# Performance work log

Hardware: AMD Instinct MI355X
Metric: run time of the kernel (lower is better)

The kernel has to match this reference:

```python
import jax, jax.numpy as jnp
import numpy as np

B, S, HID = 4, 2048, 512
NH, HD = 8, 64
MAX_REL = 512


def setup_inputs() -> dict:
    key = jax.random.key(0)
    ks = jax.random.split(key, 10)
    sd = 0.02
    return {
        "hidden_states": jax.random.normal(ks[0], (B, S, HID), jnp.float32),
        "attention_mask": jnp.ones((B, S), jnp.float32),
        "Wq": jax.random.normal(ks[1], (HID, HID), jnp.float32) * sd,
        "bq": jnp.zeros((HID,), jnp.float32),
        "Wk": jax.random.normal(ks[2], (HID, HID), jnp.float32) * sd,
        "bk": jnp.zeros((HID,), jnp.float32),
        "Wv": jax.random.normal(ks[3], (HID, HID), jnp.float32) * sd,
        "bv": jnp.zeros((HID,), jnp.float32),
        "Wo": jax.random.normal(ks[4], (HID, HID), jnp.float32) * sd,
        "bo": jnp.zeros((HID,), jnp.float32),
        "rel_table": jax.random.normal(ks[5], (2 * MAX_REL + 1, NH), jnp.float32) * sd,
    }


def _heads(x):
    # [B,S,HID] -> [B,NH,S,HD]
    return x.reshape(B, S, NH, HD).transpose(0, 2, 1, 3)


def reference(hidden_states, attention_mask, Wq, bq, Wk, bk, Wv, bv, Wo, bo, rel_table):
    q = _heads(hidden_states @ Wq + bq)
    k = _heads(hidden_states @ Wk + bk)
    v = _heads(hidden_states @ Wv + bv)

    scores = jnp.einsum("bhqd,bhkd->bhqk", q, k) / jnp.sqrt(jnp.float32(HD))

    # relative position bias: rel[i,j] = clip(j-i, -MAX_REL, MAX_REL) + MAX_REL
    pos = jnp.arange(S)
    rel = jnp.clip(pos[None, :] - pos[:, None], -MAX_REL, MAX_REL) + MAX_REL
    bias = rel_table[rel]                      # [S,S,NH]
    bias = bias.transpose(2, 0, 1)             # [NH,S,S]
    scores = scores + bias[None]

    # mask: 1 attend, 0 masked
    neg = jnp.finfo(scores.dtype).min
    scores = scores + (1.0 - attention_mask)[:, None, None, :] * neg

    probs = jax.nn.softmax(scores, axis=-1)
    ctx = jnp.einsum("bhqk,bhkd->bhqd", probs, v)
    ctx = ctx.transpose(0, 2, 1, 3).reshape(B, S, HID)
    return ctx @ Wo + bo
```

## Files before the change

### kernel.cpp

```cpp
#include <hip/hip_runtime.h>
#include <hip/hip_bf16.h>

#define B_    4
#define S_    2048
#define HID_  512
#define NH_   8
#define HD_   64
#define MAXREL 512
#define M_    (B_ * S_)

#define LOG2E 1.44269504f
#define SCALE_Q (0.125f * LOG2E)

typedef __attribute__((ext_vector_type(8))) short bf8;
typedef __attribute__((ext_vector_type(4))) float f4;
typedef __attribute__((ext_vector_type(16))) float f16f;

static __device__ __forceinline__ unsigned short f2bf(float f) {
    union { float f; unsigned int u; } v; v.f = f;
    unsigned int u = v.u;
    unsigned int r = (u + 0x7FFFu + ((u >> 16) & 1u)) >> 16;
    return (unsigned short)r;
}

static __device__ __forceinline__ float ex2(float x) {
    float r; asm("v_exp_f32 %0, %1" : "=v"(r) : "v"(x)); return r;
}

static __device__ __forceinline__ void gload16(const void* g, void* l) {
    __builtin_amdgcn_global_load_lds(
        (const __attribute__((address_space(1))) unsigned int*)g,
        (__attribute__((address_space(3))) unsigned int*)l, 16, 0, 0);
}

static __device__ __forceinline__ bf8 mkbf8(unsigned a, unsigned b, unsigned c, unsigned d) {
    uint4 u = make_uint4(a, b, c, d);
    return *(bf8*)&u;
}

#define MFMA16(a, b, c) __builtin_amdgcn_mfma_f32_16x16x32_bf16((a), (b), (c), 0, 0, 0)
#define MFMA32(a, b, c) __builtin_amdgcn_mfma_f32_32x32x16_bf16((a), (b), (c), 0, 0, 0)

__global__ void k_cast_hs(const float* __restrict__ src, unsigned short* __restrict__ dst, int n4) {
    int i = blockIdx.x * blockDim.x + threadIdx.x;
    if (i >= n4) return;
    float4 v = ((const float4*)src)[i];
    ushort4 o;
    o.x = f2bf(v.x); o.y = f2bf(v.y); o.z = f2bf(v.z); o.w = f2bf(v.w);
    ((ushort4*)dst)[i] = o;
}

__global__ void k_prep_mask(const float* __restrict__ mask, float* __restrict__ maskadd) {
    int i = blockIdx.x * blockDim.x + threadIdx.x;
    if (i < M_) maskadd[i] = (1.0f - mask[i]) * -3.0e38f;
}

__global__ void k_transpose_w4(const float* __restrict__ W0, const float* __restrict__ W1,
                               const float* __restrict__ W2, const float* __restrict__ W3,
                               unsigned short* __restrict__ T0, unsigned short* __restrict__ T1,
                               unsigned short* __restrict__ T2, unsigned short* __restrict__ T3) {
    __shared__ float tile[32][33];
    const int z = blockIdx.z;
    const float* W = (z == 0) ? W0 : (z == 1) ? W1 : (z == 2) ? W2 : W3;
    unsigned short* T = (z == 0) ? T0 : (z == 1) ? T1 : (z == 2) ? T2 : T3;
    const int tx = threadIdx.x & 31, ty = threadIdx.x >> 5;
    const int n0 = blockIdx.x * 32, k0 = blockIdx.y * 32;
    #pragma unroll
    for (int i = 0; i < 4; ++i)
        tile[ty + i * 8][tx] = W[(size_t)(k0 + ty + i * 8) * HID_ + n0 + tx];
    __syncthreads();
    #pragma unroll
    for (int i = 0; i < 4; ++i)
        T[(size_t)(n0 + ty + i * 8) * HID_ + k0 + tx] = f2bf(tile[tx][ty + i * 8]);
}

__global__ __launch_bounds__(256, 3) void k_gemm_qkv(
    const unsigned short* __restrict__ Abf,
    const unsigned short* __restrict__ Wqt, const unsigned short* __restrict__ Wkt,
    const unsigned short* __restrict__ Wvt,
    const float* __restrict__ bq, const float* __restrict__ bk, const float* __restrict__ bv,
    unsigned short* __restrict__ Q, unsigned short* __restrict__ K, unsigned short* __restrict__ Vt)
{
    __shared__ unsigned short Al[2][128 * 32];
    __shared__ unsigned short Bl[2][128 * 32];

    const int t = threadIdx.x;
    const int lane = t & 63, w = t >> 6;
    const int lr = lane & 15, lg = lane >> 4;
    const int wr = w >> 1, wc = w & 1;

    const int m0 = blockIdx.x * 128;
    const int ng = blockIdx.y * 128;
    const int z = ng >> 9;
    const int n0 = ng & 511;
    const unsigned short* Wt = (z == 0) ? Wqt : ((z == 1) ? Wkt : Wvt);
    const float* bias = (z == 0) ? bq : ((z == 1) ? bk : bv);
    const float osc = (z == 0) ? SCALE_Q : 1.0f;

    const int srow = t >> 2;
    const int sc = (((t & 3) ^ ((srow >> 1) & 3))) * 8;
    const unsigned short* Ag0 = &Abf[(size_t)(m0 + srow) * HID_ + sc];
    const unsigned short* Ag1 = &Abf[(size_t)(m0 + 64 + srow) * HID_ + sc];
    const unsigned short* Bg0 = &Wt[(size_t)(n0 + srow) * HID_ + sc];
    const unsigned short* Bg1 = &Wt[(size_t)(n0 + 64 + srow) * HID_ + sc];
    char* dA0 = (char*)&Al[0][0] + w * 1024;
    char* dB0 = (char*)&Bl[0][0] + w * 1024;

    const int fx = (lr >> 1) & 3;
    int aoff[4], boff[4];
    #pragma unroll
    for (int i = 0; i < 4; ++i) {
        aoff[i] = (wr * 64 + i * 16 + lr) * 32 + ((lg ^ fx) * 8);
        boff[i] = (wc * 64 + i * 16 + lr) * 32 + ((lg ^ fx) * 8);
    }

    gload16(Ag0, dA0);
    gload16(Ag1, dA0 + 4096);
    gload16(Bg0, dB0);
    gload16(Bg1, dB0 + 4096);
    __syncthreads();

    f4 acc[4][4] = {};
    for (int kt = 0; kt < 16; ++kt) {
        const int cur = kt & 1;
        if (kt < 15) {
            const int ko = (kt + 1) * 32;
            const int bo = (cur ^ 1) * 8192;
            gload16(Ag0 + ko, dA0 + bo);
            gload16(Ag1 + ko, dA0 + bo + 4096);
            gload16(Bg0 + ko, dB0 + bo);
            gload16(Bg1 + ko, dB0 + bo + 4096);
        }
        bf8 af[4], bf_[4];
        #pragma unroll
        for (int i = 0; i < 4; ++i) {
            af[i]  = *(const bf8*)&Al[cur][aoff[i]];
            bf_[i] = *(const bf8*)&Bl[cur][boff[i]];
        }
        #pragma unroll
        for (int mi = 0; mi < 4; ++mi)
            #pragma unroll
            for (int ni = 0; ni < 4; ++ni)
                acc[mi][ni] = MFMA16(af[mi], bf_[ni], acc[mi][ni]);
        __syncthreads();
    }

    #pragma unroll
    for (int mi = 0; mi < 4; ++mi)
    #pragma unroll
    for (int ni = 0; ni < 4; ++ni) {
        const int col = n0 + wc * 64 + ni * 16 + lr;
        const int h = col >> 6, d = col & 63;
        const float bs = bias[col];
        const int row0 = m0 + wr * 64 + mi * 16 + lg * 4;
        const int b = row0 >> 11, s0 = row0 & 2047;
        if (z == 2) {
            ushort4 o;
            o.x = f2bf(acc[mi][ni][0] + bs);
            o.y = f2bf(acc[mi][ni][1] + bs);
            o.z = f2bf(acc[mi][ni][2] + bs);
            o.w = f2bf(acc[mi][ni][3] + bs);
            *(ushort4*)&Vt[(((size_t)(b * NH_ + h)) * HD_ + d) * S_ + s0] = o;
        } else {
            unsigned short* dst = (z == 0) ? Q : K;
            #pragma unroll
            for (int r = 0; r < 4; ++r) {
                float v = (acc[mi][ni][r] + bs) * osc;
                dst[(((size_t)(b * NH_ + h)) * S_ + s0 + r) * HD_ + d] = f2bf(v);
            }
        }
    }
}

__global__ __launch_bounds__(512) void k_gemm_out(
    const unsigned short* __restrict__ Abf,
    const unsigned short* __restrict__ Wot,
    const float* __restrict__ bo,
    float* __restrict__ out)
{
    __shared__ unsigned short Al[2][128 * 32];
    __shared__ unsigned short Bl[2][128 * 32];

    const int t = threadIdx.x;
    const int lane = t & 63, w = t >> 6;
    const int lr = lane & 15, lg = lane >> 4;
    const int wr = w >> 2, wc = w & 3;

    const int m0 = blockIdx.x * 128;
    const int n0 = blockIdx.y * 128;

    const int srow = t >> 2;
    const int sc = (((t & 3) ^ ((srow >> 1) & 3))) * 8;
    const unsigned short* Ag = &Abf[(size_t)(m0 + srow) * HID_ + sc];
    const unsigned short* Bg = &Wot[(size_t)(n0 + srow) * HID_ + sc];
    char* dA = (char*)&Al[0][0] + w * 1024;
    char* dB = (char*)&Bl[0][0] + w * 1024;

    const int fx = (lr >> 1) & 3;
    int aoff[4], boff[2];
    #pragma unroll
    for (int i = 0; i < 4; ++i)
        aoff[i] = (wr * 64 + i * 16 + lr) * 32 + ((lg ^ fx) * 8);
    #pragma unroll
    for (int i = 0; i < 2; ++i)
        boff[i] = (wc * 32 + i * 16 + lr) * 32 + ((lg ^ fx) * 8);

    gload16(Ag, dA);
    gload16(Bg, dB);
    __syncthreads();

    f4 acc[4][2] = {};
    for (int kt = 0; kt < 16; ++kt) {
        const int cur = kt & 1;
        if (kt < 15) {
            const int ko = (kt + 1) * 32;
            const int bo_ = (cur ^ 1) * 8192;
            gload16(Ag + ko, dA + bo_);
            gload16(Bg + ko, dB + bo_);
        }
        bf8 af[4], bf_[2];
        #pragma unroll
        for (int i = 0; i < 4; ++i) af[i] = *(const bf8*)&Al[cur][aoff[i]];
        #pragma unroll
        for (int i = 0; i < 2; ++i) bf_[i] = *(const bf8*)&Bl[cur][boff[i]];
        #pragma unroll
        for (int mi = 0; mi < 4; ++mi)
            #pragma unroll
            for (int ni = 0; ni < 2; ++ni)
                acc[mi][ni] = MFMA16(af[mi], bf_[ni], acc[mi][ni]);
        __syncthreads();
    }

    #pragma unroll
    for (int mi = 0; mi < 4; ++mi)
    #pragma unroll
    for (int ni = 0; ni < 2; ++ni) {
        const int col = n0 + wc * 32 + ni * 16 + lr;
        const float bs = bo[col];
        const int row0 = m0 + wr * 64 + mi * 16 + lg * 4;
        #pragma unroll
        for (int r = 0; r < 4; ++r)
            out[(size_t)(row0 + r) * HID_ + col] = acc[mi][ni][r] + bs;
    }
}

__global__ __launch_bounds__(512, 4) void k_flash(
    const unsigned short* __restrict__ Q, const unsigned short* __restrict__ K,
    const unsigned short* __restrict__ Vt,
    const float* __restrict__ rel_table, const float* __restrict__ maskadd,
    unsigned short* __restrict__ ctx)
{
    __shared__ unsigned short KV[3][8192];
    __shared__ float Tw[1216];
    __shared__ float maskc[S_];

    const int t = threadIdx.x;
    const int lane = t & 63, w = t >> 6;
    const int q = lane & 31, hi = lane >> 5;
    const int g = w & 3, kvh = w >> 2;

    const int flat = blockIdx.x;
    const int idx = flat >> 3;
    const int bh = (flat & 7) * 4 + (idx >> 4);
    const int qb = idx & 15;
    const int b = bh >> 3, h = bh & 7;
    const int q0 = qb * 128;

    for (int i = t; i < 1216; i += 512) {
        int r = i - 606;
        r = r < -MAXREL ? -MAXREL : (r > MAXREL ? MAXREL : r);
        Tw[i] = rel_table[(r + MAXREL) * NH_ + h] * LOG2E;
    }
    {
        const float4* src = (const float4*)(maskadd + b * S_);
        float4* dst = (float4*)maskc;
        for (int i = t; i < S_ / 4; i += 512) dst[i] = src[i];
    }
    const float TbLo = rel_table[h] * LOG2E;
    const float TbHi = rel_table[2 * MAXREL * NH_ + h] * LOG2E;

    const unsigned short* Kb = K + (size_t)bh * S_ * HD_;
    const unsigned short* Vb = Vt + (size_t)bh * HD_ * S_;

    const int myq = q0 + g * 32 + q;
    const int qw = q0 + g * 32;
    bf8 qf[4];
    #pragma unroll
    for (int s = 0; s < 4; ++s)
        qf[s] = *(const bf8*)&Q[((size_t)bh * S_ + myq) * HD_ + s * 16 + hi * 8];

    const int srow = t >> 3, sslot = t & 7;
    const int sxor = (sslot ^ (srow & 7)) * 8;
    const size_t kb0 = (size_t)srow * HD_ + sxor;
    const size_t vb0 = (size_t)srow * S_ + sxor;
    const int woff = w * 1024;

    auto stage = [&](int kvt, int buf) {
        char* base = (char*)&KV[buf][0];
        gload16(&Kb[kb0 + (size_t)kvt * 64 * HD_], base + woff);
        gload16(&Vb[vb0 + (size_t)kvt * 64], base + 8192 + woff);
    };

    f16f ca0 = {}, ca1 = {};
    float m_s = -INFINITY, lsum = 0.f;

    stage(0, 0);
    stage(1, 1);
    asm volatile("s_waitcnt lgkmcnt(0)" ::: "memory");
    asm volatile("s_waitcnt vmcnt(2)" ::: "memory");
    __builtin_amdgcn_s_barrier();
    __builtin_amdgcn_sched_barrier(0);

    const int xq = q & 7;
    const int jb0 = 606 + 32 * kvh + 4 * hi - q0 - g * 32 - q;
    for (int ti = 0; ti < 32; ++ti) {
        const int kv0 = ti * 64;
        const int cur = ti % 3;
        const int kvs = kv0 + 32 * kvh;

        if (ti < 30) stage(ti + 2, (ti + 2) % 3);

        const unsigned short* Kt  = &KV[cur][0];
        const unsigned short* Vtl = &KV[cur][4096];

        f16f sa = {};
        __builtin_amdgcn_s_setprio(1);
        #pragma unroll
        for (int s = 0; s < 4; ++s) {
            bf8 kf = *(const bf8*)&Kt[(32 * kvh + q) * 64 + (((2 * s + hi) ^ xq) * 8)];
            sa = MFMA32(kf, qf[s], sa);
        }
        __builtin_amdgcn_s_setprio(0);

        float t0 = -INFINITY, t1 = -INFINITY, t2 = -INFINITY, t3 = -INFINITY;
        {
            const bool ulo = (kvs + 31 - qw <= -MAXREL);
            const bool uhi = (kvs - (qw + 31) >= MAXREL);
            if (ulo || uhi) {
                const float bc = ulo ? TbLo : TbHi;
                #pragma unroll
                for (int m = 0; m < 4; ++m) {
                    float4 mk = *(const float4*)&maskc[kvs + m * 8 + hi * 4];
                    float s0 = sa[4 * m + 0] + bc + mk.x;  sa[4 * m + 0] = s0;  t0 = fmaxf(t0, s0);
                    float s1 = sa[4 * m + 1] + bc + mk.y;  sa[4 * m + 1] = s1;  t1 = fmaxf(t1, s1);
                    float s2 = sa[4 * m + 2] + bc + mk.z;  sa[4 * m + 2] = s2;  t2 = fmaxf(t2, s2);
                    float s3 = sa[4 * m + 3] + bc + mk.w;  sa[4 * m + 3] = s3;  t3 = fmaxf(t3, s3);
                }
            } else {
                #pragma unroll
                for (int m = 0; m < 4; ++m) {
                    float4 mk = *(const float4*)&maskc[kvs + m * 8 + hi * 4];
                    const int jb = jb0 + kv0 + m * 8;
                    float s0 = sa[4 * m + 0] + Tw[jb + 0] + mk.x;  sa[4 * m + 0] = s0;  t0 = fmaxf(t0, s0);
                    float s1 = sa[4 * m + 1] + Tw[jb + 1] + mk.y;  sa[4 * m + 1] = s1;  t1 = fmaxf(t1, s1);
                    float s2 = sa[4 * m + 2] + Tw[jb + 2] + mk.z;  sa[4 * m + 2] = s2;  t2 = fmaxf(t2, s2);
                    float s3 = sa[4 * m + 3] + Tw[jb + 3] + mk.w;  sa[4 * m + 3] = s3;  t3 = fmaxf(t3, s3);
                }
            }
        }
        float tmaxl = fmaxf(fmaxf(t0, t1), fmaxf(t2, t3));
        const float tmax = fmaxf(tmaxl, __shfl_xor(tmaxl, 32));

        float ptile = 0.f;
        unsigned int pk[8];
        #pragma unroll
        for (int m = 0; m < 4; ++m) {
            float a0 = ex2(sa[4 * m + 0] - m_s), a1 = ex2(sa[4 * m + 1] - m_s);
            float a2 = ex2(sa[4 * m + 2] - m_s), a3 = ex2(sa[4 * m + 3] - m_s);
            ptile += (a0 + a1) + (a2 + a3);
            asm("v_cvt_pk_bf16_f32 %0, %1, %2" : "=v"(pk[2 * m])     : "v"(a0), "v"(a1));
            asm("v_cvt_pk_bf16_f32 %0, %1, %2" : "=v"(pk[2 * m + 1]) : "v"(a2), "v"(a3));
        }
        if (!__all(tmax <= m_s + 8.0f)) {
            const float mnew = fmaxf(m_s, tmax);
            const float fac = ex2(m_s - mnew);
            lsum *= fac;
            ca0 *= fac;
            ca1 *= fac;
            ptile = 0.f;
            #pragma unroll
            for (int m = 0; m < 4; ++m) {
                float a0 = ex2(sa[4 * m + 0] - mnew), a1 = ex2(sa[4 * m + 1] - mnew);
                float a2 = ex2(sa[4 * m + 2] - mnew), a3 = ex2(sa[4 * m + 3] - mnew);
                ptile += (a0 + a1) + (a2 + a3);
                asm("v_cvt_pk_bf16_f32 %0, %1, %2" : "=v"(pk[2 * m])     : "v"(a0), "v"(a1));
                asm("v_cvt_pk_bf16_f32 %0, %1, %2" : "=v"(pk[2 * m + 1]) : "v"(a2), "v"(a3));
            }
            m_s = mnew;
        }
        lsum += ptile;

        bf8 pf0, pf1;
        {
            unsigned c0 = pk[0], c2 = pk[2], c1 = pk[1], c3 = pk[3];
            asm("v_permlane32_swap_b32 %0, %1" : "+v"(c0), "+v"(c2));
            asm("v_permlane32_swap_b32 %0, %1" : "+v"(c1), "+v"(c3));
            pf0 = mkbf8(c0, c1, c2, c3);
        }
        {
            unsigned c0 = pk[4], c2 = pk[6], c1 = pk[5], c3 = pk[7];
            asm("v_permlane32_swap_b32 %0, %1" : "+v"(c0), "+v"(c2));
            asm("v_permlane32_swap_b32 %0, %1" : "+v"(c1), "+v"(c3));
            pf1 = mkbf8(c0, c1, c2, c3);
        }

        __builtin_amdgcn_s_setprio(1);
        #pragma unroll
        for (int s = 0; s < 2; ++s) {
            const int slot = ((4 * kvh + 2 * s + hi) ^ xq) * 8;
            bf8 v0 = *(const bf8*)&Vtl[q * 64 + slot];
            bf8 v1 = *(const bf8*)&Vtl[(q + 32) * 64 + slot];
            bf8 pf = (s == 0) ? pf0 : pf1;
            ca0 = MFMA32(v0, pf, ca0);
            ca1 = MFMA32(v1, pf, ca1);
        }
        __builtin_amdgcn_s_setprio(0);

        if (ti < 31) {
            if (ti < 30) asm volatile("s_waitcnt vmcnt(2)" ::: "memory");
            else         asm volatile("s_waitcnt vmcnt(0)" ::: "memory");
            __builtin_amdgcn_s_barrier();
            __builtin_amdgcn_sched_barrier(0);
        }
    }

    lsum += __shfl_xor(lsum, 32);

    __syncthreads();
    float* mg = (float*)&KV[0][0];
    if (kvh == 1) {
        const int base = g * 34 * 64;
        #pragma unroll
        for (int j = 0; j < 16; ++j) mg[base + j * 64 + lane] = ca0[j];
        #pragma unroll
        for (int j = 0; j < 16; ++j) mg[base + (16 + j) * 64 + lane] = ca1[j];
        mg[base + 32 * 64 + lane] = m_s;
        mg[base + 33 * 64 + lane] = lsum;
    }
    __syncthreads();
    if (kvh == 0) {
        const int base = g * 34 * 64;
        const float pm = mg[base + 32 * 64 + lane];
        const float pl = mg[base + 33 * 64 + lane];
        const float mm = fmaxf(m_s, pm);
        const float fa = ex2(m_s - mm);
        const float fb = ex2(pm - mm);
        const float lm = lsum * fa + pl * fb;
        const float inv = 1.0f / lm;
        unsigned short* cg = &ctx[(size_t)(b * S_ + myq) * HID_ + h * HD_];
        #pragma unroll
        for (int m = 0; m < 4; ++m) {
            ushort4 o0;
            o0.x = f2bf((ca0[4 * m + 0] * fa + mg[base + (4 * m + 0) * 64 + lane] * fb) * inv);
            o0.y = f2bf((ca0[4 * m + 1] * fa + mg[base + (4 * m + 1) * 64 + lane] * fb) * inv);
            o0.z = f2bf((ca0[4 * m + 2] * fa + mg[base + (4 * m + 2) * 64 + lane] * fb) * inv);
            o0.w = f2bf((ca0[4 * m + 3] * fa + mg[base + (4 * m + 3) * 64 + lane] * fb) * inv);
            *(ushort4*)&cg[m * 8 + hi * 4] = o0;
            ushort4 o1;
            o1.x = f2bf((ca1[4 * m + 0] * fa + mg[base + (16 + 4 * m + 0) * 64 + lane] * fb) * inv);
            o1.y = f2bf((ca1[4 * m + 1] * fa + mg[base + (16 + 4 * m + 1) * 64 + lane] * fb) * inv);
            o1.z = f2bf((ca1[4 * m + 2] * fa + mg[base + (16 + 4 * m + 2) * 64 + lane] * fb) * inv);
            o1.w = f2bf((ca1[4 * m + 3] * fa + mg[base + (16 + 4 * m + 3) * 64 + lane] * fb) * inv);
            *(ushort4*)&cg[32 + m * 8 + hi * 4] = o1;
        }
    }
}

extern "C" void kernel_launch(void* const* d_in, const int* in_sizes, int n_in,
                              void* d_out, int out_size, void* d_ws, size_t ws_size,
                              hipStream_t stream) {
    const float* hs  = (const float*)d_in[0];
    const float* msk = (const float*)d_in[1];
    const float* Wq  = (const float*)d_in[2];
    const float* bq  = (const float*)d_in[3];
    const float* Wk  = (const float*)d_in[4];
    const float* bk  = (const float*)d_in[5];
    const float* Wv  = (const float*)d_in[6];
    const float* bv  = (const float*)d_in[7];
    const float* Wo  = (const float*)d_in[8];
    const float* bo  = (const float*)d_in[9];
    const float* rel = (const float*)d_in[10];
    float* out = (float*)d_out;

    char* ws = (char*)d_ws;
    unsigned short* hsb = (unsigned short*)ws; ws += (size_t)M_ * HID_ * 2;
    unsigned short* Wqt = (unsigned short*)ws; ws += (size_t)HID_ * HID_ * 2;
    unsigned short* Wkt = (unsigned short*)ws; ws += (size_t)HID_ * HID_ * 2;
    unsigned short* Wvt = (unsigned short*)ws; ws += (size_t)HID_ * HID_ * 2;
    unsigned short* Wot = (unsigned short*)ws; ws += (size_t)HID_ * HID_ * 2;
    unsigned short* Qb  = (unsigned short*)ws; ws += (size_t)M_ * HID_ * 2;
    unsigned short* Kb  = (unsigned short*)ws; ws += (size_t)M_ * HID_ * 2;
    unsigned short* Vtb = (unsigned short*)ws; ws += (size_t)M_ * HID_ * 2;
    unsigned short* ctxb= (unsigned short*)ws; ws += (size_t)M_ * HID_ * 2;
    float* maskadd      = (float*)ws;          ws += (size_t)M_ * 4;

    k_cast_hs<<<(M_ * HID_ / 4 + 255) / 256, 256, 0, stream>>>(hs, hsb, M_ * HID_ / 4);
    k_prep_mask<<<(M_ + 255) / 256, 256, 0, stream>>>(msk, maskadd);
    k_transpose_w4<<<dim3(16, 16, 4), 256, 0, stream>>>(Wq, Wk, Wv, Wo, Wqt, Wkt, Wvt, Wot);
    k_gemm_qkv<<<dim3(64, 12), 256, 0, stream>>>(
        hsb, Wqt, Wkt, Wvt, bq, bk, bv, Qb, Kb, Vtb);
    k_flash<<<512, 512, 0, stream>>>(Qb, Kb, Vtb, rel, maskadd, ctxb);
    k_gemm_out<<<dim3(64, 4), 512, 0, stream>>>(ctxb, Wot, bo, out);
}
```

Before: 110.5 us.

## Pack attention mask into bitmask words and skip mask adds for unmasked tiles

Replaces the per-element float additive mask with a 32-bit-per-word bitmask computed inside the cast kernel, which removes the separate mask-prep launch. In the flash kernel each lane holds one mask word, fetched via readlane per KV tile. The mask add is skipped when a tile is fully unmasked, which drops the 8KB LDS mask buffer and the per-tile LDS reads. This cuts LDS traffic and VALU adds in the softmax inner loop and frees LDS for occupancy, at the cost of a branch and a single block doing the serial mask packing. Mask semantics change slightly: the threshold is now >0.5 instead of an additive (1-mask)*min, so fractional masks are treated differently.

Measured after the change: 105.1 us (median of 2 runs). -4.9%, faster.

```diff
diff --git a/kernel.cpp b/kernel.cpp
--- a/kernel.cpp
+++ b/kernel.cpp
@@ -41,18 +41,24 @@
 #define MFMA16(a, b, c) __builtin_amdgcn_mfma_f32_16x16x32_bf16((a), (b), (c), 0, 0, 0)
 #define MFMA32(a, b, c) __builtin_amdgcn_mfma_f32_32x32x16_bf16((a), (b), (c), 0, 0, 0)
 
-__global__ void k_cast_hs(const float* __restrict__ src, unsigned short* __restrict__ dst, int n4) {
+__global__ void k_cast_hs(const float* __restrict__ src, unsigned short* __restrict__ dst, int n4,
+                          const float* __restrict__ mask, unsigned* __restrict__ maskbits) {
     int i = blockIdx.x * blockDim.x + threadIdx.x;
-    if (i >= n4) return;
-    float4 v = ((const float4*)src)[i];
-    ushort4 o;
-    o.x = f2bf(v.x); o.y = f2bf(v.y); o.z = f2bf(v.z); o.w = f2bf(v.w);
-    ((ushort4*)dst)[i] = o;
-}
-
-__global__ void k_prep_mask(const float* __restrict__ mask, float* __restrict__ maskadd) {
-    int i = blockIdx.x * blockDim.x + threadIdx.x;
-    if (i < M_) maskadd[i] = (1.0f - mask[i]) * -3.0e38f;
+    if (i < n4) {
+        float4 v = ((const float4*)src)[i];
+        ushort4 o;
+        o.x = f2bf(v.x); o.y = f2bf(v.y); o.z = f2bf(v.z); o.w = f2bf(v.w);
+        ((ushort4*)dst)[i] = o;
+    }
+    if (blockIdx.x == 0 && threadIdx.x < 256) {
+        const int t = threadIdx.x;
+        const int b = t >> 6, wd = t & 63;
+        unsigned bits = 0;
+        #pragma unroll
+        for (int j = 0; j < 32; ++j)
+            bits |= (mask[b * S_ + wd * 32 + j] > 0.5f ? 1u : 0u) << j;
+        maskbits[t] = bits;
+    }
 }
 
 __global__ void k_transpose_w4(const float* __restrict__ W0, const float* __restrict__ W1,
@@ -247,12 +253,11 @@
 __global__ __launch_bounds__(512, 4) void k_flash(
     const unsigned short* __restrict__ Q, const unsigned short* __restrict__ K,
     const unsigned short* __restrict__ Vt,
-    const float* __restrict__ rel_table, const float* __restrict__ maskadd,
+    const float* __restrict__ rel_table, const unsigned* __restrict__ maskbits,
     unsigned short* __restrict__ ctx)
 {
     __shared__ unsigned short KV[3][8192];
     __shared__ float Tw[1216];
-    __shared__ float maskc[S_];
 
     const int t = threadIdx.x;
     const int lane = t & 63, w = t >> 6;
@@ -266,15 +271,13 @@
     const int b = bh >> 3, h = bh & 7;
     const int q0 = qb * 128;
 
+    unsigned mword = 0xFFFFFFFFu;
+    if (lane < 32) mword = maskbits[b * 64 + 2 * lane + kvh];
+
     for (int i = t; i < 1216; i += 512) {
         int r = i - 606;
         r = r < -MAXREL ? -MAXREL : (r > MAXREL ? MAXREL : r);
         Tw[i] = rel_table[(r + MAXREL) * NH_ + h] * LOG2E;
-    }
-    {
-        const float4* src = (const float4*)(maskadd + b * S_);
-        float4* dst = (float4*)maskc;
-        for (int i = t; i < S_ / 4; i += 512) dst[i] = src[i];
     }
     const float TbLo = rel_table[h] * LOG2E;
     const float TbHi = rel_table[2 * MAXREL * NH_ + h] * LOG2E;
@@ -331,6 +334,17 @@
             sa = MFMA32(kf, qf[s], sa);
         }
         __builtin_amdgcn_s_setprio(0);
+
+        const unsigned mws = __builtin_amdgcn_readlane(mword, ti);
+        if (mws != 0xFFFFFFFFu) {
+            #pragma unroll
+            for (int m = 0; m < 4; ++m) {
+                const unsigned tb = mws >> (8 * m + 4 * hi);
+                #pragma unroll
+                for (int r = 0; r < 4; ++r)
+                    sa[4 * m + r] += ((tb >> r) & 1) ? 0.f : -3.0e38f;
+            }
+        }
 
         float t0 = -INFINITY, t1 = -INFINITY, t2 = -INFINITY, t3 = -INFINITY;
         {
@@ -340,21 +354,19 @@
                 const float bc = ulo ? TbLo : TbHi;
                 #pragma unroll
                 for (int m = 0; m < 4; ++m) {
-                    float4 mk = *(const float4*)&maskc[kvs + m * 8 + hi * 4];
-                    float s0 = sa[4 * m + 0] + bc + mk.x;  sa[4 * m + 0] = s0;  t0 = fmaxf(t0, s0);
-                    float s1 = sa[4 * m + 1] + bc + mk.y;  sa[4 * m + 1] = s1;  t1 = fmaxf(t1, s1);
-                    float s2 = sa[4 * m + 2] + bc + mk.z;  sa[4 * m + 2] = s2;  t2 = fmaxf(t2, s2);
-                    float s3 = sa[4 * m + 3] + bc + mk.w;  sa[4 * m + 3] = s3;  t3 = fmaxf(t3, s3);
+                    float s0 = sa[4 * m + 0] + bc;  sa[4 * m + 0] = s0;  t0 = fmaxf(t0, s0);
+                    float s1 = sa[4 * m + 1] + bc;  sa[4 * m + 1] = s1;  t1 = fmaxf(t1, s1);
+                    float s2 = sa[4 * m + 2] + bc;  sa[4 * m + 2] = s2;  t2 = fmaxf(t2, s2);
+                    float s3 = sa[4 * m + 3] + bc;  sa[4 * m + 3] = s3;  t3 = fmaxf(t3, s3);
                 }
             } else {
                 #pragma unroll
                 for (int m = 0; m < 4; ++m) {
-                    float4 mk = *(const float4*)&maskc[kvs + m * 8 + hi * 4];
                     const int jb = jb0 + kv0 + m * 8;
-                    float s0 = sa[4 * m + 0] + Tw[jb + 0] + mk.x;  sa[4 * m + 0] = s0;  t0 = fmaxf(t0, s0);
-                    float s1 = sa[4 * m + 1] + Tw[jb + 1] + mk.y;  sa[4 * m + 1] = s1;  t1 = fmaxf(t1, s1);
-                    float s2 = sa[4 * m + 2] + Tw[jb + 2] + mk.z;  sa[4 * m + 2] = s2;  t2 = fmaxf(t2, s2);
-                    float s3 = sa[4 * m + 3] + Tw[jb + 3] + mk.w;  sa[4 * m + 3] = s3;  t3 = fmaxf(t3, s3);
+                    float s0 = sa[4 * m + 0] + Tw[jb + 0];  sa[4 * m + 0] = s0;  t0 = fmaxf(t0, s0);
+                    float s1 = sa[4 * m + 1] + Tw[jb + 1];  sa[4 * m + 1] = s1;  t1 = fmaxf(t1, s1);
+                    float s2 = sa[4 * m + 2] + Tw[jb + 2];  sa[4 * m + 2] = s2;  t2 = fmaxf(t2, s2);
+                    float s3 = sa[4 * m + 3] + Tw[jb + 3];  sa[4 * m + 3] = s3;  t3 = fmaxf(t3, s3);
                 }
             }
         }
@@ -492,13 +504,13 @@
     unsigned short* Kb  = (unsigned short*)ws; ws += (size_t)M_ * HID_ * 2;
     unsigned short* Vtb = (unsigned short*)ws; ws += (size_t)M_ * HID_ * 2;
     unsigned short* ctxb= (unsigned short*)ws; ws += (size_t)M_ * HID_ * 2;
-    float* maskadd      = (float*)ws;          ws += (size_t)M_ * 4;
-
-    k_cast_hs<<<(M_ * HID_ / 4 + 255) / 256, 256, 0, stream>>>(hs, hsb, M_ * HID_ / 4);
-    k_prep_mask<<<(M_ + 255) / 256, 256, 0, stream>>>(msk, maskadd);
+    unsigned* maskbits  = (unsigned*)ws;       ws += (size_t)B_ * 64 * 4;
+
+    k_cast_hs<<<(M_ * HID_ / 4 + 255) / 256, 256, 0, stream>>>(
+        hs, hsb, M_ * HID_ / 4, msk, maskbits);
     k_transpose_w4<<<dim3(16, 16, 4), 256, 0, stream>>>(Wq, Wk, Wv, Wo, Wqt, Wkt, Wvt, Wot);
     k_gemm_qkv<<<dim3(64, 12), 256, 0, stream>>>(
         hsb, Wqt, Wkt, Wvt, bq, bk, bv, Qb, Kb, Vtb);
-    k_flash<<<512, 512, 0, stream>>>(Qb, Kb, Vtb, rel, maskadd, ctxb);
+    k_flash<<<512, 512, 0, stream>>>(Qb, Kb, Vtb, rel, maskbits, ctxb);
     k_gemm_out<<<dim3(64, 4), 512, 0, stream>>>(ctxb, Wot, bo, out);
 }
```
